# Optimization experiments

Hardware: AMD Instinct MI355X
Metric: run time of the kernel (lower is better)

## Reference

```python
import jax, jax.numpy as jnp
import numpy as np

DIM = 1024
CTX_DIM = 1024
VALUE_DIM = 1024
HEADS = 16
HEAD_DIM = DIM // HEADS        # q/k head dim = 64
V_HEAD_DIM = VALUE_DIM // HEADS
LN_EPS = 1e-5


def setup_inputs() -> dict:
    key = jax.random.key(0)
    k0, k1, k2, k3, k4 = jax.random.split(key, 5)
    B, N, M = 4, 1024, 1024
    x = jax.random.normal(k0, (B, N, DIM), jnp.float32)
    context = jax.random.normal(k1, (B, M, CTX_DIM), jnp.float32)
    # Linear weights stored as [in, out] (y = x @ W), matching torch Linear math
    Wq = jax.random.normal(k2, (DIM, DIM), jnp.float32) * (DIM ** -0.5)
    Wkv = jax.random.normal(k3, (CTX_DIM, DIM + VALUE_DIM), jnp.float32) * (CTX_DIM ** -0.5)
    Wt = jax.random.normal(k4, (HEADS, HEADS), jnp.float32) * (HEADS ** -0.5)
    gamma = jnp.ones((HEADS,), jnp.float32)
    beta = jnp.zeros((HEADS,), jnp.float32)
    return {"x": x, "context": context, "Wq": Wq, "Wkv": Wkv,
            "Wt": Wt, "gamma": gamma, "beta": beta}


def reference(x, context, Wq, Wkv, Wt, gamma, beta):
    B, N, _ = x.shape
    M = context.shape[1]
    # projections
    q = (x @ Wq).reshape(B, N, HEADS, HEAD_DIM).transpose(0, 2, 1, 3)       # [B,H,N,d]
    kv = context @ Wkv                                                      # [B,M,dim+vdim]
    k = kv[..., :DIM].reshape(B, M, HEADS, HEAD_DIM).transpose(0, 2, 1, 3)  # [B,H,M,d]
    v = kv[..., DIM:].reshape(B, M, HEADS, V_HEAD_DIM).transpose(0, 2, 1, 3)
    # scaled dot-product scores, fully materialized as in the original
    scale = HEAD_DIM ** -0.5
    dots = jnp.einsum('bhid,bhjd->bhij', q * scale, k)                      # [B,H,N,M]
    w = jax.nn.softmax(dots, axis=-1)
    # talking heads: Linear(heads,heads,bias=False) then LayerNorm(heads) over head axis
    w = jnp.einsum('bhij,hg->bgij', w, Wt)
    mu = jnp.mean(w, axis=1, keepdims=True)
    var = jnp.var(w, axis=1, keepdims=True)
    w = (w - mu) * jax.lax.rsqrt(var + LN_EPS)
    w = w * gamma[None, :, None, None] + beta[None, :, None, None]
    attn = jnp.einsum('bhij,bhjd->bhid', w, v)                              # [B,H,N,vd]
    out = attn.transpose(0, 2, 1, 3).reshape(B, N, VALUE_DIM)
    return out
```

## Files before the change

### kernel.cpp

```cpp
#include <hip/hip_runtime.h>
#include <hip/hip_bf16.h>

typedef __bf16 bf16;
typedef bf16 bf16x2 __attribute__((ext_vector_type(2)));
typedef bf16 bf16x4 __attribute__((ext_vector_type(4)));
typedef bf16 bf16x8 __attribute__((ext_vector_type(8)));
typedef float floatx4 __attribute__((ext_vector_type(4)));

#define MFMA_BF16(a, b, c) __builtin_amdgcn_mfma_f32_16x16x32_bf16((a), (b), (c), 0, 0, 0)

__global__ __launch_bounds__(256) void cvt_kernel(const float* __restrict__ in,
                                                  bf16* __restrict__ out, int n8) {
    int idx = blockIdx.x * 256 + threadIdx.x;
    if (idx >= n8) return;
    const float* src = in + (size_t)idx * 8;
    float4 f0 = *(const float4*)src;
    float4 f1 = *(const float4*)(src + 4);
    bf16x8 v = {(bf16)f0.x, (bf16)f0.y, (bf16)f0.z, (bf16)f0.w,
                (bf16)f1.x, (bf16)f1.y, (bf16)f1.z, (bf16)f1.w};
    *(bf16x8*)(out + (size_t)idx * 8) = v;
}

__global__ __launch_bounds__(256) void trans_kernel(const float* __restrict__ in,
                                                    bf16* __restrict__ out, int R, int C) {
    __shared__ float tile[32][33];
    const int t = threadIdx.x;
    const int r0 = blockIdx.y * 32, c0 = blockIdx.x * 32;
    int r = t >> 3, c4 = (t & 7) * 4;
    float4 v = *(const float4*)&in[(size_t)(r0 + r) * C + c0 + c4];
    tile[r][c4 + 0] = v.x; tile[r][c4 + 1] = v.y;
    tile[r][c4 + 2] = v.z; tile[r][c4 + 3] = v.w;
    __syncthreads();
    int rp = t >> 3, cp = (t & 7) * 4;
    bf16x4 w = {(bf16)tile[cp + 0][rp], (bf16)tile[cp + 1][rp],
                (bf16)tile[cp + 2][rp], (bf16)tile[cp + 3][rp]};
    *(bf16x4*)&out[(size_t)(c0 + rp) * R + r0 + cp] = w;
}

__global__ __launch_bounds__(256) void vtrans_kernel(const bf16* __restrict__ in,
                                                     bf16* __restrict__ out) {
    __shared__ bf16 tile[32][36];
    const int t = threadIdx.x;
    const int r0 = blockIdx.y * 32, c0 = blockIdx.x * 32;
    int r = t >> 3, c4 = (t & 7) * 4;
    bf16x4 v = *(const bf16x4*)&in[(size_t)(r0 + r) * 1024 + c0 + c4];
    tile[r][c4 + 0] = v[0]; tile[r][c4 + 1] = v[1];
    tile[r][c4 + 2] = v[2]; tile[r][c4 + 3] = v[3];
    __syncthreads();
    int rp = t >> 3, cp = (t & 7) * 4;
    int hd = c0 + rp;
    int b = r0 >> 10, j = (r0 & 1023) + cp;
    bf16x4 w = {tile[cp + 0][rp], tile[cp + 1][rp], tile[cp + 2][rp], tile[cp + 3][rp]};
    *(bf16x4*)&out[(size_t)(b * 1024 + hd) * 1024 + j] = w;
}

template <int MODE>
__global__ __launch_bounds__(256) void gemm128(const bf16* __restrict__ A,
                                               const bf16* __restrict__ B,
                                               bf16* __restrict__ C,
                                               bf16* __restrict__ V, int N) {
    __shared__ bf16 As[128 * 40];
    __shared__ bf16 Bs[128 * 40];
    const int t = threadIdx.x;
    const int wv = t >> 6, lane = t & 63, quad = lane >> 4, l15 = lane & 15;
    const int wr = wv >> 1, wc = wv & 1;
    const int m0 = blockIdx.y * 128, n0 = blockIdx.x * 128;
    const int ra = t >> 1, kc = (t & 1) * 16;

    floatx4 acc[4][4] = {};

    for (int k0 = 0; k0 < 1024; k0 += 32) {
        bf16x8 a0 = *(const bf16x8*)&A[(size_t)(m0 + ra) * 1024 + k0 + kc];
        bf16x8 a1 = *(const bf16x8*)&A[(size_t)(m0 + ra) * 1024 + k0 + kc + 8];
        bf16x8 b0 = *(const bf16x8*)&B[(size_t)(n0 + ra) * 1024 + k0 + kc];
        bf16x8 b1 = *(const bf16x8*)&B[(size_t)(n0 + ra) * 1024 + k0 + kc + 8];
        __syncthreads();
        *(bf16x8*)&As[ra * 40 + kc] = a0;
        *(bf16x8*)&As[ra * 40 + kc + 8] = a1;
        *(bf16x8*)&Bs[ra * 40 + kc] = b0;
        *(bf16x8*)&Bs[ra * 40 + kc + 8] = b1;
        __syncthreads();
        bf16x8 af[4], bfr[4];
#pragma unroll
        for (int mt = 0; mt < 4; ++mt)
            af[mt] = *(bf16x8*)&As[(wr * 64 + mt * 16 + l15) * 40 + quad * 8];
#pragma unroll
        for (int nt = 0; nt < 4; ++nt)
            bfr[nt] = *(bf16x8*)&Bs[(wc * 64 + nt * 16 + l15) * 40 + quad * 8];
#pragma unroll
        for (int mt = 0; mt < 4; ++mt)
#pragma unroll
            for (int nt = 0; nt < 4; ++nt)
                acc[mt][nt] = MFMA_BF16(af[mt], bfr[nt], acc[mt][nt]);
    }
#pragma unroll
    for (int mt = 0; mt < 4; ++mt)
#pragma unroll
        for (int nt = 0; nt < 4; ++nt)
#pragma unroll
            for (int r = 0; r < 4; ++r) {
                int m = m0 + wr * 64 + mt * 16 + quad * 4 + r;
                int n = n0 + wc * 64 + nt * 16 + l15;
                bf16 val = (bf16)acc[mt][nt][r];
                if (MODE == 0) {
                    C[(size_t)m * N + n] = val;
                } else {
                    if (n < 1024) C[(size_t)m * 1024 + n] = val;
                    else          V[(size_t)m * 1024 + (n - 1024)] = val;
                }
            }
}

__global__ __launch_bounds__(256) void denom_kernel(const bf16* __restrict__ Qb,
                                                    const bf16* __restrict__ Kb,
                                                    float* __restrict__ L) {
    const int t = threadIdx.x;
    const int wv = t >> 6, lane = t & 63, quad = lane >> 4, l15 = lane & 15;
    const int i0 = blockIdx.x * 32, b = blockIdx.y, jz = blockIdx.z;
    const float scale = 0.125f;

    bf16x8 qa[4][2][2];
#pragma unroll
    for (int hh = 0; hh < 4; ++hh)
#pragma unroll
        for (int it = 0; it < 2; ++it) {
            const bf16* qp = Qb + (size_t)(b * 1024 + i0 + it * 16 + l15) * 1024 +
                             (wv * 4 + hh) * 64 + quad * 8;
            qa[hh][it][0] = *(const bf16x8*)qp;
            qa[hh][it][1] = *(const bf16x8*)(qp + 32);
        }
    floatx4 se[4][2] = {};
    const bf16* Kbase = Kb + (size_t)b * 1024 * 1024;

    for (int jt = 0; jt < 16; ++jt) {
        int j = jz * 256 + jt * 16 + l15;
#pragma unroll
        for (int hh = 0; hh < 4; ++hh) {
            const bf16* kp = Kbase + (size_t)j * 1024 + (wv * 4 + hh) * 64 + quad * 8;
            bf16x8 k0 = *(const bf16x8*)kp;
            bf16x8 k1 = *(const bf16x8*)(kp + 32);
#pragma unroll
            for (int it = 0; it < 2; ++it) {
                floatx4 c = {0.f, 0.f, 0.f, 0.f};
                c = MFMA_BF16(qa[hh][it][0], k0, c);
                c = MFMA_BF16(qa[hh][it][1], k1, c);
#pragma unroll
                for (int r = 0; r < 4; ++r) se[hh][it][r] += __expf(c[r] * scale);
            }
        }
    }
#pragma unroll
    for (int hh = 0; hh < 4; ++hh)
#pragma unroll
        for (int it = 0; it < 2; ++it)
#pragma unroll
            for (int r = 0; r < 4; ++r) {
                float s = se[hh][it][r];
                s += __shfl_xor(s, 1); s += __shfl_xor(s, 2);
                s += __shfl_xor(s, 4); s += __shfl_xor(s, 8);
                if (l15 == 0)
                    atomicAdd(&L[(size_t)(b * 16 + wv * 4 + hh) * 1024 + i0 + it * 16 +
                                 quad * 4 + r], s);
            }
}

__global__ __launch_bounds__(512, 4) void attn_kernel(const bf16* __restrict__ Qb,
                                                      const bf16* __restrict__ Kb,
                                                      const bf16* __restrict__ Vt,
                                                      const float* __restrict__ L,
                                                      const float* __restrict__ Wt,
                                                      const float* __restrict__ gamma,
                                                      const float* __restrict__ beta,
                                                      float* __restrict__ out) {
    __shared__ bf16 Buf1[512 * 20];
    __shared__ bf16 Buf2[16 * 648];
    __shared__ __align__(16) bf16 Zbuf[8];

    const int t = threadIdx.x;
    const int wv = t >> 6, lane = t & 63, quad = lane >> 4, l15 = lane & 15;
    const int i0 = blockIdx.x * 16, b = blockIdx.y, jz = blockIdx.z;
    const float scale = 0.125f;

    if (t < 8) Zbuf[t] = (bf16)0.f;

    bf16x8 a_wt;
#pragma unroll
    for (int jj = 0; jj < 8; ++jj) {
        int k = quad * 8 + jj;
        float v = 0.f;
        if (k < 16) {
            float s = 0.f;
            for (int g = 0; g < 16; ++g) s += Wt[k * 16 + g];
            v = Wt[k * 16 + l15] - s * 0.0625f;
        }
        a_wt[jj] = (bf16)v;
    }
    float gq[4], bq[4];
#pragma unroll
    for (int r = 0; r < 4; ++r) { gq[r] = gamma[quad * 4 + r]; bq[r] = beta[quad * 4 + r]; }

    bf16x8 qa[2][2];
    float invl[2][4];
#pragma unroll
    for (int hh = 0; hh < 2; ++hh) {
        int h = wv * 2 + hh;
        const bf16* qp = Qb + (size_t)(b * 1024 + i0 + l15) * 1024 + h * 64 + quad * 8;
        qa[hh][0] = *(const bf16x8*)qp;
        qa[hh][1] = *(const bf16x8*)(qp + 32);
#pragma unroll
        for (int r = 0; r < 4; ++r)
            invl[hh][r] = 1.f / L[(size_t)(b * 16 + h) * 1024 + i0 + quad * 4 + r];
    }

    const bf16* Kbase = Kb + (size_t)b * 1024 * 1024;
    const bf16* Vbase = Vt + (size_t)b * 16 * 64 * 1024;
    floatx4 o[2][4] = {};

    for (int jt = 0; jt < 16; ++jt) {
        const int j0 = jz * 512 + jt * 32;
#pragma unroll
        for (int ns = 0; ns < 2; ++ns) {
            floatx4 cw[2];
#pragma unroll
            for (int hh = 0; hh < 2; ++hh) {
                int h = wv * 2 + hh;
                const bf16* kp = Kbase + (size_t)(j0 + ns * 16 + l15) * 1024 + h * 64 + quad * 8;
                floatx4 c = {0.f, 0.f, 0.f, 0.f};
                c = MFMA_BF16(qa[hh][0], *(const bf16x8*)kp, c);
                c = MFMA_BF16(qa[hh][1], *(const bf16x8*)(kp + 32), c);
                cw[hh] = c;
            }
#pragma unroll
            for (int r = 0; r < 4; ++r) {
                bf16x2 pk = {(bf16)(__expf(cw[0][r] * scale) * invl[0][r]),
                             (bf16)(__expf(cw[1][r] * scale) * invl[1][r])};
                *(bf16x2*)&Buf1[((quad * 4 + r) * 32 + ns * 16 + l15) * 20 + wv * 2] = pk;
            }
        }
        __syncthreads();
#pragma unroll
        for (int grp = 0; grp < 4; ++grp) {
            int gi = wv * 4 + grp, ig = gi >> 1, jb = (gi & 1) * 16;
            int p = ig * 32 + jb + l15;
            const bf16* src = (quad < 2) ? &Buf1[p * 20 + quad * 8] : Zbuf;
            floatx4 c = {0.f, 0.f, 0.f, 0.f};
            c = MFMA_BF16(a_wt, *(const bf16x8*)src, c);
            float s2 = c[0] * c[0] + c[1] * c[1] + c[2] * c[2] + c[3] * c[3];
            s2 += __shfl_xor(s2, 16);
            s2 += __shfl_xor(s2, 32);
            float rs = rsqrtf(s2 * 0.0625f + 1e-5f);
#pragma unroll
            for (int r = 0; r < 4; ++r) {
                float w2 = c[r] * rs * gq[r] + bq[r];
                Buf2[(quad * 4 + r) * 648 + ig * 40 + jb + l15] = (bf16)w2;
            }
        }
        __syncthreads();
#pragma unroll
        for (int hh = 0; hh < 2; ++hh) {
            int g = wv * 2 + hh;
            bf16x8 a = *(bf16x8*)&Buf2[g * 648 + l15 * 40 + quad * 8];
#pragma unroll
            for (int dt = 0; dt < 4; ++dt) {
                const bf16* vp = Vbase + (size_t)(g * 64 + dt * 16 + l15) * 1024 + j0 + quad * 8;
                o[hh][dt] = MFMA_BF16(a, *(const bf16x8*)vp, o[hh][dt]);
            }
        }
    }
#pragma unroll
    for (int hh = 0; hh < 2; ++hh) {
        int g = wv * 2 + hh;
#pragma unroll
        for (int dt = 0; dt < 4; ++dt)
#pragma unroll
            for (int r = 0; r < 4; ++r)
                atomicAdd(&out[(size_t)(b * 1024 + i0 + quad * 4 + r) * 1024 +
                               g * 64 + dt * 16 + l15], o[hh][dt][r]);
    }
}

extern "C" void kernel_launch(void* const* d_in, const int* in_sizes, int n_in,
                              void* d_out, int out_size, void* d_ws, size_t ws_size,
                              hipStream_t stream) {
    const float* x     = (const float*)d_in[0];
    const float* ctx   = (const float*)d_in[1];
    const float* Wq    = (const float*)d_in[2];
    const float* Wkv   = (const float*)d_in[3];
    const float* Wt    = (const float*)d_in[4];
    const float* gamma = (const float*)d_in[5];
    const float* beta  = (const float*)d_in[6];
    float* out = (float*)d_out;

    bf16* xb   = (bf16*)d_ws;
    bf16* cb   = xb + (size_t)4 * 1024 * 1024;
    bf16* WqT  = cb + (size_t)4 * 1024 * 1024;
    bf16* WkvT = WqT + (size_t)1024 * 1024;
    bf16* Qb   = WkvT + (size_t)2048 * 1024;
    bf16* Kb   = Qb + (size_t)4 * 1024 * 1024;
    bf16* Vr   = Kb + (size_t)4 * 1024 * 1024;
    bf16* Vt   = Vr + (size_t)4 * 1024 * 1024;
    float* L   = (float*)(Vt + (size_t)4 * 1024 * 1024);

    hipMemsetAsync(L, 0, (size_t)4 * 16 * 1024 * sizeof(float), stream);
    hipMemsetAsync(out, 0, (size_t)out_size * sizeof(float), stream);

    cvt_kernel<<<2048, 256, 0, stream>>>(x, xb, 524288);
    cvt_kernel<<<2048, 256, 0, stream>>>(ctx, cb, 524288);
    trans_kernel<<<dim3(32, 32), 256, 0, stream>>>(Wq, WqT, 1024, 1024);
    trans_kernel<<<dim3(64, 32), 256, 0, stream>>>(Wkv, WkvT, 1024, 2048);

    gemm128<0><<<dim3(8, 32), 256, 0, stream>>>(xb, WqT, Qb, nullptr, 1024);
    gemm128<1><<<dim3(16, 32), 256, 0, stream>>>(cb, WkvT, Kb, Vr, 2048);
    vtrans_kernel<<<dim3(32, 128), 256, 0, stream>>>(Vr, Vt);

    denom_kernel<<<dim3(32, 4, 4), 256, 0, stream>>>(Qb, Kb, L);
    attn_kernel<<<dim3(64, 4, 2), 512, 0, stream>>>(Qb, Kb, Vt, L, Wt, gamma, beta, out);
}
```

Before: 356.2 us.

## Split key range finer, precompute talking-heads weights, and pad LDS to avoid conflicts

Both the denominator and attention kernels now split the key dimension into more chunks (16 and 4 instead of 4 and 2), giving more blocks for better occupancy, and launch bounds are raised. A tiny prep kernel computes the mean-centered, transposed talking-heads weight once into scratch (reusing the Vr buffer after the V transpose), so each attention block no longer recomputes it. The Buf2 layout gets an XOR-like offset instead of 648 padding to reduce LDS bank conflicts and shrink shared memory. The cost is more atomic adds into L and the output.

```diff
diff --git a/kernel.cpp b/kernel.cpp
--- a/kernel.cpp
+++ b/kernel.cpp
@@ -52,6 +52,17 @@
     int b = r0 >> 10, j = (r0 & 1023) + cp;
     bf16x4 w = {tile[cp + 0][rp], tile[cp + 1][rp], tile[cp + 2][rp], tile[cp + 3][rp]};
     *(bf16x4*)&out[(size_t)(b * 1024 + hd) * 1024 + j] = w;
+}
+
+__global__ __launch_bounds__(256) void prep_wt_kernel(const float* __restrict__ Wt,
+                                                      bf16* __restrict__ WtcT) {
+    const int t = threadIdx.x;
+    const int g = t >> 4, k = t & 15;
+    float s = 0.f;
+#pragma unroll
+    for (int gg = 0; gg < 16; ++gg) s += Wt[k * 16 + gg];
+    WtcT[g * 32 + k] = (bf16)(Wt[k * 16 + g] - s * 0.0625f);
+    WtcT[g * 32 + 16 + k] = (bf16)0.f;
 }
 
 template <int MODE>
@@ -111,90 +122,74 @@
             }
 }
 
-__global__ __launch_bounds__(256) void denom_kernel(const bf16* __restrict__ Qb,
-                                                    const bf16* __restrict__ Kb,
-                                                    float* __restrict__ L) {
+__global__ __launch_bounds__(256, 8) void denom_kernel(const bf16* __restrict__ Qb,
+                                                       const bf16* __restrict__ Kb,
+                                                       float* __restrict__ L) {
     const int t = threadIdx.x;
     const int wv = t >> 6, lane = t & 63, quad = lane >> 4, l15 = lane & 15;
     const int i0 = blockIdx.x * 32, b = blockIdx.y, jz = blockIdx.z;
     const float scale = 0.125f;
-
-    bf16x8 qa[4][2][2];
-#pragma unroll
-    for (int hh = 0; hh < 4; ++hh)
+    const bf16* Kbase = Kb + (size_t)b * 1024 * 1024;
+
+    for (int hh = 0; hh < 4; ++hh) {
+        const int h = wv * 4 + hh;
+        bf16x8 qa[2][2];
 #pragma unroll
         for (int it = 0; it < 2; ++it) {
             const bf16* qp = Qb + (size_t)(b * 1024 + i0 + it * 16 + l15) * 1024 +
-                             (wv * 4 + hh) * 64 + quad * 8;
-            qa[hh][it][0] = *(const bf16x8*)qp;
-            qa[hh][it][1] = *(const bf16x8*)(qp + 32);
-        }
-    floatx4 se[4][2] = {};
-    const bf16* Kbase = Kb + (size_t)b * 1024 * 1024;
-
-    for (int jt = 0; jt < 16; ++jt) {
-        int j = jz * 256 + jt * 16 + l15;
-#pragma unroll
-        for (int hh = 0; hh < 4; ++hh) {
-            const bf16* kp = Kbase + (size_t)j * 1024 + (wv * 4 + hh) * 64 + quad * 8;
+                             h * 64 + quad * 8;
+            qa[it][0] = *(const bf16x8*)qp;
+            qa[it][1] = *(const bf16x8*)(qp + 32);
+        }
+        floatx4 se[2] = {};
+#pragma unroll
+        for (int jt = 0; jt < 4; ++jt) {
+            int j = jz * 64 + jt * 16 + l15;
+            const bf16* kp = Kbase + (size_t)j * 1024 + h * 64 + quad * 8;
             bf16x8 k0 = *(const bf16x8*)kp;
             bf16x8 k1 = *(const bf16x8*)(kp + 32);
 #pragma unroll
             for (int it = 0; it < 2; ++it) {
                 floatx4 c = {0.f, 0.f, 0.f, 0.f};
-                c = MFMA_BF16(qa[hh][it][0], k0, c);
-                c = MFMA_BF16(qa[hh][it][1], k1, c);
-#pragma unroll
-                for (int r = 0; r < 4; ++r) se[hh][it][r] += __expf(c[r] * scale);
-            }
-        }
-    }
-#pragma unroll
-    for (int hh = 0; hh < 4; ++hh)
+                c = MFMA_BF16(qa[it][0], k0, c);
+                c = MFMA_BF16(qa[it][1], k1, c);
+#pragma unroll
+                for (int r = 0; r < 4; ++r) se[it][r] += __expf(c[r] * scale);
+            }
+        }
 #pragma unroll
         for (int it = 0; it < 2; ++it)
 #pragma unroll
             for (int r = 0; r < 4; ++r) {
-                float s = se[hh][it][r];
+                float s = se[it][r];
                 s += __shfl_xor(s, 1); s += __shfl_xor(s, 2);
                 s += __shfl_xor(s, 4); s += __shfl_xor(s, 8);
                 if (l15 == 0)
-                    atomicAdd(&L[(size_t)(b * 16 + wv * 4 + hh) * 1024 + i0 + it * 16 +
+                    atomicAdd(&L[(size_t)(b * 16 + h) * 1024 + i0 + it * 16 +
                                  quad * 4 + r], s);
             }
-}
-
-__global__ __launch_bounds__(512, 4) void attn_kernel(const bf16* __restrict__ Qb,
+    }
+}
+
+__global__ __launch_bounds__(512, 8) void attn_kernel(const bf16* __restrict__ Qb,
                                                       const bf16* __restrict__ Kb,
                                                       const bf16* __restrict__ Vt,
                                                       const float* __restrict__ L,
-                                                      const float* __restrict__ Wt,
+                                                      const bf16* __restrict__ WtcT,
                                                       const float* __restrict__ gamma,
                                                       const float* __restrict__ beta,
                                                       float* __restrict__ out) {
     __shared__ bf16 Buf1[512 * 20];
-    __shared__ bf16 Buf2[16 * 648];
-    __shared__ __align__(16) bf16 Zbuf[8];
-
+    __shared__ bf16 Buf2[16 * 640];
     const int t = threadIdx.x;
     const int wv = t >> 6, lane = t & 63, quad = lane >> 4, l15 = lane & 15;
     const int i0 = blockIdx.x * 16, b = blockIdx.y, jz = blockIdx.z;
     const float scale = 0.125f;
 
-    if (t < 8) Zbuf[t] = (bf16)0.f;
-
-    bf16x8 a_wt;
-#pragma unroll
-    for (int jj = 0; jj < 8; ++jj) {
-        int k = quad * 8 + jj;
-        float v = 0.f;
-        if (k < 16) {
-            float s = 0.f;
-            for (int g = 0; g < 16; ++g) s += Wt[k * 16 + g];
-            v = Wt[k * 16 + l15] - s * 0.0625f;
-        }
-        a_wt[jj] = (bf16)v;
-    }
+    if (t < 8) Buf2[2560 + t] = (bf16)0.f;
+    const bf16* Zbuf = &Buf2[2560];
+
+    bf16x8 a_wt = *(const bf16x8*)&WtcT[l15 * 32 + quad * 8];
     float gq[4], bq[4];
 #pragma unroll
     for (int r = 0; r < 4; ++r) { gq[r] = gamma[quad * 4 + r]; bq[r] = beta[quad * 4 + r]; }
@@ -216,8 +211,8 @@
     const bf16* Vbase = Vt + (size_t)b * 16 * 64 * 1024;
     floatx4 o[2][4] = {};
 
-    for (int jt = 0; jt < 16; ++jt) {
-        const int j0 = jz * 512 + jt * 32;
+    for (int jt = 0; jt < 8; ++jt) {
+        const int j0 = jz * 256 + jt * 32;
 #pragma unroll
         for (int ns = 0; ns < 2; ++ns) {
             floatx4 cw[2];
@@ -252,14 +247,14 @@
 #pragma unroll
             for (int r = 0; r < 4; ++r) {
                 float w2 = c[r] * rs * gq[r] + bq[r];
-                Buf2[(quad * 4 + r) * 648 + ig * 40 + jb + l15] = (bf16)w2;
+                Buf2[(quad * 4 + r) * 640 + (quad & 1) * 8 + ig * 40 + jb + l15] = (bf16)w2;
             }
         }
         __syncthreads();
 #pragma unroll
         for (int hh = 0; hh < 2; ++hh) {
             int g = wv * 2 + hh;
-            bf16x8 a = *(bf16x8*)&Buf2[g * 648 + l15 * 40 + quad * 8];
+            bf16x8 a = *(bf16x8*)&Buf2[g * 640 + ((g >> 2) & 1) * 8 + l15 * 40 + quad * 8];
 #pragma unroll
             for (int dt = 0; dt < 4; ++dt) {
                 const bf16* vp = Vbase + (size_t)(g * 64 + dt * 16 + l15) * 1024 + j0 + quad * 8;
@@ -300,6 +295,7 @@
     bf16* Vr   = Kb + (size_t)4 * 1024 * 1024;
     bf16* Vt   = Vr + (size_t)4 * 1024 * 1024;
     float* L   = (float*)(Vt + (size_t)4 * 1024 * 1024);
+    bf16* WtcT = Vr;
 
     hipMemsetAsync(L, 0, (size_t)4 * 16 * 1024 * sizeof(float), stream);
     hipMemsetAsync(out, 0, (size_t)out_size * sizeof(float), stream);
@@ -312,7 +308,8 @@
     gemm128<0><<<dim3(8, 32), 256, 0, stream>>>(xb, WqT, Qb, nullptr, 1024);
     gemm128<1><<<dim3(16, 32), 256, 0, stream>>>(cb, WkvT, Kb, Vr, 2048);
     vtrans_kernel<<<dim3(32, 128), 256, 0, stream>>>(Vr, Vt);
-
-    denom_kernel<<<dim3(32, 4, 4), 256, 0, stream>>>(Qb, Kb, L);
-    attn_kernel<<<dim3(64, 4, 2), 512, 0, stream>>>(Qb, Kb, Vt, L, Wt, gamma, beta, out);
-}
+    prep_wt_kernel<<<1, 256, 0, stream>>>(Wt, WtcT);
+
+    denom_kernel<<<dim3(32, 4, 16), 256, 0, stream>>>(Qb, Kb, L);
+    attn_kernel<<<dim3(64, 4, 4), 512, 0, stream>>>(Qb, Kb, Vt, L, WtcT, gamma, beta, out);
+}
```

Result: slower. 550.8 us (+54.6%).
